# Optimization experiments

Measured on AMD Instinct MI355X. Metric: run time of the kernel, lower is better.

Reference implementation:

```python
import jax, jax.numpy as jnp
import numpy as np

D = 128   # hidden_dims
H = 8     # head_num
ALPHA = 0.5
EPS = 1e-5


def setup_inputs() -> dict:
    key = jax.random.key(0)
    ks = jax.random.split(key, 16)
    B, S = 2, 2048
    s = 0.02
    inp = {
        'x': jax.random.normal(ks[0], (B, S, D), jnp.float32),
        'adj_matrix': jax.random.randint(ks[1], (S, S), 0, 2, jnp.int32),
        'Wq': jax.random.normal(ks[2], (D, D * H), jnp.float32) * s,
        'bq': jnp.zeros((D * H,), jnp.float32),
        'Wk': jax.random.normal(ks[3], (D, D * H), jnp.float32) * s,
        'bk': jnp.zeros((D * H,), jnp.float32),
        'Wv': jax.random.normal(ks[4], (D, D * H), jnp.float32) * s,
        'bv': jnp.zeros((D * H,), jnp.float32),
        'Wo': jax.random.normal(ks[5], (D * H, D), jnp.float32) * s,
        'bo': jnp.zeros((D,), jnp.float32),
        'g1': jnp.ones((D,), jnp.float32), 'be1': jnp.zeros((D,), jnp.float32),
        'g2': jnp.ones((D,), jnp.float32), 'be2': jnp.zeros((D,), jnp.float32),
        'W1': jax.random.normal(ks[6], (D, D), jnp.float32) * s,
        'b1': jnp.zeros((D,), jnp.float32),
        'W2': jax.random.normal(ks[7], (D, D), jnp.float32) * s,
        'b2': jnp.zeros((D,), jnp.float32),
    }
    return inp


def _layernorm(x, g, b):
    mu = jnp.mean(x, axis=-1, keepdims=True)
    var = jnp.var(x, axis=-1, keepdims=True)
    return (x - mu) * jax.lax.rsqrt(var + EPS) * g + b


def reference(x, adj_matrix, Wq, bq, Wk, bk, Wv, bv, Wo, bo, g1, be1, g2, be2, W1, b1, W2, b2):
    B, S, _ = x.shape
    q = (x @ Wq + bq).reshape(B, S, H, D)
    k = (x @ Wk + bk).reshape(B, S, H, D)
    v = (x @ Wv + bv).reshape(B, S, H, D)
    scores = jnp.einsum('bqhd,bkhd->bhqk', q, k) / jnp.sqrt(jnp.float32(D))
    soft_mask = ALPHA * adj_matrix.astype(jnp.float32) + (1.0 - ALPHA)  # [S,S]
    scores = scores * soft_mask  # broadcast over B,H
    attn = jax.nn.softmax(scores, axis=-1)
    out = jnp.einsum('bhqk,bkhd->bqhd', attn, v).reshape(B, S, H * D)
    out = out @ Wo + bo
    h = _layernorm(x + out, g1, be1)
    ff = jax.nn.relu(h @ W1 + b1) @ W2 + b2
    y = _layernorm(h + ff, g2, be2)
    return y, attn
```

## Files before the change

kernel.cpp:

```cpp
#include <hip/hip_runtime.h>
#include <hip/hip_bf16.h>

#define HD 128
#define NH 8
#define SQ 2048
#define NROWS 4096
#define QSCALE 0.06375871607f

typedef __bf16 bf16;
typedef bf16 bf16x8 __attribute__((ext_vector_type(8)));
typedef float f32x4 __attribute__((ext_vector_type(4)));

__device__ __forceinline__ f32x4 mfma16(bf16x8 a, bf16x8 b, f32x4 c) {
  return __builtin_amdgcn_mfma_f32_16x16x32_bf16(a, b, c, 0, 0, 0);
}
__device__ __forceinline__ bf16x8 ld8(const bf16* p) { return *(const bf16x8*)p; }
__device__ __forceinline__ unsigned short bfu(float v) {
  return __builtin_bit_cast(unsigned short, (bf16)v);
}
__device__ __forceinline__ unsigned packbf2(float a, float b) {
  return (unsigned)bfu(a) | ((unsigned)bfu(b) << 16);
}
__device__ __forceinline__ void gload_lds16(const void* g, void* l) {
  __builtin_amdgcn_global_load_lds(
      (const __attribute__((address_space(1))) void*)g,
      (__attribute__((address_space(3))) void*)l, 16, 0, 0);
}

__global__ void k_prep_a(const float* __restrict__ x, const int* __restrict__ adj,
                         bf16* __restrict__ xb, unsigned char* __restrict__ mask8) {
  int idx = blockIdx.x * 256 + threadIdx.x;
  if (idx < NROWS * HD) { xb[idx] = (bf16)x[idx]; return; }
  int j = idx - NROWS * HD;
  if (j < (SQ * SQ / 4)) {
    int4 a = ((const int4*)adj)[j];
    uchar4 m;
    m.x = (unsigned char)a.x; m.y = (unsigned char)a.y;
    m.z = (unsigned char)a.z; m.w = (unsigned char)a.w;
    ((uchar4*)mask8)[j] = m;
  }
}

__global__ void k_prep_w(const float* __restrict__ Wq, const float* __restrict__ Wk,
                         const float* __restrict__ Wv, const float* __restrict__ Wo,
                         const float* __restrict__ W1, const float* __restrict__ W2,
                         bf16* __restrict__ WqkvT, bf16* __restrict__ WoT,
                         bf16* __restrict__ W1T, bf16* __restrict__ W2T) {
  int idx = blockIdx.x * 256 + threadIdx.x;
  if (idx < 3072 * 128) {
    int n = idx >> 7, kk = idx & 127;
    int sel = n >> 10, nn = n & 1023;
    const float* W = (sel == 0) ? Wq : (sel == 1 ? Wk : Wv);
    WqkvT[idx] = (bf16)W[kk * 1024 + nn];
    return;
  }
  int j = idx - 3072 * 128;
  if (j < 128 * 1024) { int n = j >> 10, kk = j & 1023; WoT[j] = (bf16)Wo[kk * 128 + n]; return; }
  j -= 128 * 1024;
  if (j < 16384) { int n = j >> 7, kk = j & 127; W1T[j] = (bf16)W1[kk * 128 + n]; return; }
  j -= 16384;
  if (j < 16384) { int n = j >> 7, kk = j & 127; W2T[j] = (bf16)W2[kk * 128 + n]; return; }
}

__global__ __launch_bounds__(256, 4) void k_qkv(
    const bf16* __restrict__ xb, const bf16* __restrict__ WqkvT,
    const float* __restrict__ bq, const float* __restrict__ bk, const float* __restrict__ bv,
    bf16* __restrict__ qT, bf16* __restrict__ kT, bf16* __restrict__ vT) {
  const int bid = blockIdx.x;
  const int m0 = (bid & 63) << 6;
  const int n0 = (bid >> 6) << 6;
  const int tid = threadIdx.x;
  const int w = tid >> 6, lane = tid & 63, lo = lane & 15, hi = lane >> 4;
  const int mw = m0 + ((w >> 1) << 5);
  const int nw = n0 + ((w & 1) << 5);
  bf16x8 av[2][4], bw[2][4];
#pragma unroll
  for (int ms = 0; ms < 2; ++ms)
#pragma unroll
    for (int ks = 0; ks < 4; ++ks)
      av[ms][ks] = ld8(xb + (size_t)(mw + ms * 16 + lo) * 128 + ks * 32 + hi * 8);
#pragma unroll
  for (int ns = 0; ns < 2; ++ns)
#pragma unroll
    for (int ks = 0; ks < 4; ++ks)
      bw[ns][ks] = ld8(WqkvT + (size_t)(nw + ns * 16 + lo) * 128 + ks * 32 + hi * 8);
  const f32x4 z4 = {0.f, 0.f, 0.f, 0.f};
  f32x4 acc[2][2] = {{z4, z4}, {z4, z4}};
#pragma unroll
  for (int ms = 0; ms < 2; ++ms)
#pragma unroll
    for (int ns = 0; ns < 2; ++ns)
#pragma unroll
      for (int ks = 0; ks < 4; ++ks)
        acc[ms][ns] = mfma16(av[ms][ks], bw[ns][ks], acc[ms][ns]);
#pragma unroll
  for (int ns = 0; ns < 2; ++ns) {
    const int n = nw + ns * 16 + lo;
    const int sel = n >> 10, nn = n & 1023;
    const float bia = (sel == 0 ? bq : sel == 1 ? bk : bv)[nn];
    const int hh = nn >> 7, d = nn & 127;
#pragma unroll
    for (int ms = 0; ms < 2; ++ms) {
      const int mb = mw + ms * 16 + hi * 4;
      const int bb = mb >> 11, s = mb & 2047;
      if (sel == 0) {
#pragma unroll
        for (int r = 0; r < 4; ++r)
          qT[(size_t)((bb * 8 + hh) * 2048 + s + r) * 128 + d] =
              (bf16)((acc[ms][ns][r] + bia) * QSCALE);
      } else if (sel == 1) {
#pragma unroll
        for (int r = 0; r < 4; ++r)
          kT[(size_t)((bb * 8 + hh) * 2048 + s + r) * 128 + d] = (bf16)(acc[ms][ns][r] + bia);
      } else {
        ushort4 pk;
        pk.x = bfu(acc[ms][ns][0] + bia);
        pk.y = bfu(acc[ms][ns][1] + bia);
        pk.z = bfu(acc[ms][ns][2] + bia);
        pk.w = bfu(acc[ms][ns][3] + bia);
        *(ushort4*)(vT + (size_t)((bb * 8 + hh) * 128 + d) * 2048 + s) = pk;
      }
    }
  }
}

__global__ __launch_bounds__(256, 2) void k_attn(
    const bf16* __restrict__ qT, const bf16* __restrict__ kT,
    const bf16* __restrict__ vT, const unsigned char* __restrict__ mask8,
    float* __restrict__ attn_out, bf16* __restrict__ Oc) {
  __shared__ __align__(16) char kbuf[2][8192];
  __shared__ __align__(16) char vbuf[2][8192];
  __shared__ __align__(16) char stash[4][1024];
  __shared__ float red2[64];

  const int lbid = blockIdx.x;
  const int work = ((lbid & 7) << 6) + (lbid >> 3);
  const int bh = work >> 5;
  const int q0 = (work & 31) << 6;
  const int b = bh >> 3, h = bh & 7;
  const int tid = threadIdx.x;
  const int w = tid >> 6, lane = tid & 63, lo = lane & 15, hi = lane >> 4;

  const bf16* Qh = qT + (size_t)bh * SQ * HD;
  const bf16* Kh = kT + (size_t)bh * SQ * HD;
  const bf16* Vh = vT + (size_t)bh * HD * SQ;
  const int qg = q0 + w * 16 + lo;

  const int krow0 = (w << 2) + (lane >> 4);
  const int krow1 = 16 + krow0;
  const bf16* kg0 = Kh + (size_t)krow0 * HD + (((lane & 15) ^ (krow0 & 7)) << 3);
  const bf16* kg1 = Kh + (size_t)krow1 * HD + (((lane & 15) ^ (krow1 & 7)) << 3);
  const int vrow0 = (w << 4) + (lane >> 2);
  const int vrow1 = 64 + vrow0;
  const bf16* vg0 = Vh + (size_t)vrow0 * SQ + ((lane & 3) << 3);
  const bf16* vg1 = Vh + (size_t)vrow1 * SQ + ((lane & 3) << 3);

  bf16x8 qf[4];
#pragma unroll
  for (int ks = 0; ks < 4; ++ks)
    qf[ks] = ld8(Qh + (size_t)qg * HD + ks * 32 + hi * 8);

  const f32x4 z4 = {0.f, 0.f, 0.f, 0.f};
  f32x4 acc[8];
#pragma unroll
  for (int ds = 0; ds < 8; ++ds) acc[ds] = z4;
  float ssum = 0.f;

  gload_lds16(kg0, &kbuf[0][w * 1024]);
  gload_lds16(kg1, &kbuf[0][4096 + w * 1024]);
  gload_lds16(vg0, &vbuf[0][w * 1024]);
  gload_lds16(vg1, &vbuf[0][4096 + w * 1024]);
  __syncthreads();

  for (int i = 0; i < 64; ++i) {
    const int kvA = i << 5;
    const int cur = i & 1;
    if (i < 63) {
      const size_t ko = (size_t)(kvA + 32) * HD;
      gload_lds16(kg0 + ko, &kbuf[cur ^ 1][w * 1024]);
      gload_lds16(kg1 + ko, &kbuf[cur ^ 1][4096 + w * 1024]);
      gload_lds16(vg0 + (kvA + 32), &vbuf[cur ^ 1][w * 1024]);
      gload_lds16(vg1 + (kvA + 32), &vbuf[cur ^ 1][4096 + w * 1024]);
    }
    const char* kb = kbuf[cur];
    const char* vb = vbuf[cur];
#pragma unroll
    for (int t = 0; t < 2; ++t) {
      const int row = t * 16 + lo;
      bf16x8 af[4];
#pragma unroll
      for (int ks = 0; ks < 4; ++ks)
        af[ks] = *(const bf16x8*)(kb + row * 256 + ((((ks << 2) + hi)) ^ (row & 7)) * 16);
      f32x4 c = z4;
#pragma unroll
      for (int ks = 0; ks < 4; ++ks) c = mfma16(af[ks], qf[ks], c);
      const unsigned mu = *(const unsigned*)(mask8 + (size_t)qg * SQ + kvA + t * 16 + hi * 4);
      float p0 = exp2f(fmaf(c[0], (float)(mu & 0xff),         c[0]));
      float p1 = exp2f(fmaf(c[1], (float)((mu >> 8) & 0xff),  c[1]));
      float p2 = exp2f(fmaf(c[2], (float)((mu >> 16) & 0xff), c[2]));
      float p3 = exp2f(fmaf(c[3], (float)((mu >> 24) & 0xff), c[3]));
      ssum += (p0 + p1) + (p2 + p3);
      *(uint2*)(stash[w] + lo * 64 + ((t * 32 + hi * 8) ^ ((lo & 3) << 4))) =
          make_uint2(packbf2(p0, p1), packbf2(p2, p3));
    }
    bf16x8 pa = *(const bf16x8*)(stash[w] + lo * 64 + ((hi * 16) ^ ((lo & 3) << 4)));
    __builtin_amdgcn_s_setprio(1);
#pragma unroll
    for (int ds = 0; ds < 8; ++ds) {
      bf16x8 vf = *(const bf16x8*)(vb + (ds * 16 + lo) * 64 + hi * 16);
      acc[ds] = mfma16(pa, vf, acc[ds]);
    }
    __builtin_amdgcn_s_setprio(0);
    __syncthreads();
  }

  ssum += __shfl_xor(ssum, 16);
  ssum += __shfl_xor(ssum, 32);
  if (hi == 0) red2[w * 16 + lo] = 1.0f / ssum;
  __syncthreads();

#pragma unroll
  for (int ds = 0; ds < 8; ++ds)
#pragma unroll
    for (int r = 0; r < 4; ++r) {
      const int qrow = w * 16 + hi * 4 + r;
      Oc[(size_t)(b * SQ + q0 + qrow) * (NH * HD) + h * HD + ds * 16 + lo] =
          (bf16)(acc[ds][r] * red2[qrow]);
    }

  const float lr = log2f(red2[w * 16 + lo]);
  float* abase = attn_out + (size_t)bh * SQ * SQ + (size_t)qg * SQ;
  gload_lds16(kg0, &kbuf[0][w * 1024]);
  gload_lds16(kg1, &kbuf[0][4096 + w * 1024]);
  __syncthreads();
  for (int i = 0; i < 64; ++i) {
    const int kvA = i << 5;
    const int cur = i & 1;
    if (i < 63) {
      const size_t ko = (size_t)(kvA + 32) * HD;
      gload_lds16(kg0 + ko, &kbuf[cur ^ 1][w * 1024]);
      gload_lds16(kg1 + ko, &kbuf[cur ^ 1][4096 + w * 1024]);
    }
    const char* kb = kbuf[cur];
#pragma unroll
    for (int t = 0; t < 2; ++t) {
      const int row = t * 16 + lo;
      bf16x8 af[4];
#pragma unroll
      for (int ks = 0; ks < 4; ++ks)
        af[ks] = *(const bf16x8*)(kb + row * 256 + ((((ks << 2) + hi)) ^ (row & 7)) * 16);
      f32x4 c = z4;
#pragma unroll
      for (int ks = 0; ks < 4; ++ks) c = mfma16(af[ks], qf[ks], c);
      const unsigned mu = *(const unsigned*)(mask8 + (size_t)qg * SQ + kvA + t * 16 + hi * 4);
      f32x4 o;
      o[0] = exp2f(fmaf(c[0], (float)(mu & 0xff),         c[0] + lr));
      o[1] = exp2f(fmaf(c[1], (float)((mu >> 8) & 0xff),  c[1] + lr));
      o[2] = exp2f(fmaf(c[2], (float)((mu >> 16) & 0xff), c[2] + lr));
      o[3] = exp2f(fmaf(c[3], (float)((mu >> 24) & 0xff), c[3] + lr));
      __builtin_nontemporal_store(o, (f32x4*)(abase + kvA + t * 16 + hi * 4));
    }
    __syncthreads();
  }
}

__global__ __launch_bounds__(256, 4) void k_owo(
    const bf16* __restrict__ Oc, const bf16* __restrict__ WoT,
    const float* __restrict__ bo, const float* __restrict__ x,
    const float* __restrict__ g1, const float* __restrict__ be1,
    float* __restrict__ hf, bf16* __restrict__ hb) {
  __shared__ __align__(16) float hbuf[16 * 128];
  const int m0 = blockIdx.x * 16;
  const int tid = threadIdx.x;
  const int w = tid >> 6, lane = tid & 63, lo = lane & 15, hi = lane >> 4;
  const int nw = w * 32;
  const f32x4 z4 = {0.f, 0.f, 0.f, 0.f};
  f32x4 acc[2] = {z4, z4};
#pragma unroll 4
  for (int kk = 0; kk < 32; ++kk) {
    bf16x8 a = ld8(Oc + (size_t)(m0 + lo) * 1024 + kk * 32 + hi * 8);
#pragma unroll
    for (int ns = 0; ns < 2; ++ns) {
      bf16x8 bb = ld8(WoT + (size_t)(nw + ns * 16 + lo) * 1024 + kk * 32 + hi * 8);
      acc[ns] = mfma16(a, bb, acc[ns]);
    }
  }
#pragma unroll
  for (int ns = 0; ns < 2; ++ns) {
    const int n = nw + ns * 16 + lo;
    const float bia = bo[n];
#pragma unroll
    for (int r = 0; r < 4; ++r) {
      const int mr = hi * 4 + r;
      hbuf[mr * 128 + n] = acc[ns][r] + bia + x[(size_t)(m0 + mr) * 128 + n];
    }
  }
  __syncthreads();
  const float2 g = *(const float2*)(g1 + lane * 2);
  const float2 be = *(const float2*)(be1 + lane * 2);
#pragma unroll
  for (int rr = 0; rr < 4; ++rr) {
    const int row = w * 4 + rr;
    float2 v = *(float2*)&hbuf[row * 128 + lane * 2];
    float s = v.x + v.y, sq = v.x * v.x + v.y * v.y;
#pragma unroll
    for (int off = 32; off; off >>= 1) { s += __shfl_xor(s, off); sq += __shfl_xor(sq, off); }
    const float mean = s * (1.f / 128.f);
    const float var = sq * (1.f / 128.f) - mean * mean;
    const float rstd = rsqrtf(var + 1e-5f);
    const float y0 = (v.x - mean) * rstd * g.x + be.x;
    const float y1 = (v.y - mean) * rstd * g.y + be.y;
    const size_t o = (size_t)(m0 + row) * 128 + lane * 2;
    *(float2*)(hf + o) = make_float2(y0, y1);
    *(unsigned*)(hb + o) = packbf2(y0, y1);
  }
}

__global__ __launch_bounds__(256, 4) void k_ffn(
    const bf16* __restrict__ hb, const float* __restrict__ hf,
    const bf16* __restrict__ W1T, const bf16* __restrict__ W2T,
    const float* __restrict__ b1, const float* __restrict__ b2,
    const float* __restrict__ g2, const float* __restrict__ be2,
    float* __restrict__ yout) {
  __shared__ __align__(16) bf16 s1[16 * 136];
  __shared__ __align__(16) float ybuf[16 * 128];
  const int m0 = blockIdx.x * 16;
  const int tid = threadIdx.x;
  const int w = tid >> 6, lane = tid & 63, lo = lane & 15, hi = lane >> 4;
  const int nw = w * 32;
  const f32x4 z4 = {0.f, 0.f, 0.f, 0.f};
  f32x4 a1[2] = {z4, z4};
#pragma unroll
  for (int kk = 0; kk < 4; ++kk) {
    bf16x8 a = ld8(hb + (size_t)(m0 + lo) * 128 + kk * 32 + hi * 8);
#pragma unroll
    for (int ns = 0; ns < 2; ++ns)
      a1[ns] = mfma16(a, ld8(W1T + (size_t)(nw + ns * 16 + lo) * 128 + kk * 32 + hi * 8), a1[ns]);
  }
#pragma unroll
  for (int ns = 0; ns < 2; ++ns) {
    const int n = nw + ns * 16 + lo;
    const float bia = b1[n];
#pragma unroll
    for (int r = 0; r < 4; ++r)
      s1[(hi * 4 + r) * 136 + n] = (bf16)fmaxf(a1[ns][r] + bia, 0.f);
  }
  __syncthreads();
  f32x4 a2[2] = {z4, z4};
#pragma unroll
  for (int kk = 0; kk < 4; ++kk) {
    bf16x8 a = *(const bf16x8*)&s1[lo * 136 + kk * 32 + hi * 8];
#pragma unroll
    for (int ns = 0; ns < 2; ++ns)
      a2[ns] = mfma16(a, ld8(W2T + (size_t)(nw + ns * 16 + lo) * 128 + kk * 32 + hi * 8), a2[ns]);
  }
#pragma unroll
  for (int ns = 0; ns < 2; ++ns) {
    const int n = nw + ns * 16 + lo;
    const float bia = b2[n];
#pragma unroll
    for (int r = 0; r < 4; ++r) {
      const int mr = hi * 4 + r;
      ybuf[mr * 128 + n] = a2[ns][r] + bia + hf[(size_t)(m0 + mr) * 128 + n];
    }
  }
  __syncthreads();
  const float2 g = *(const float2*)(g2 + lane * 2);
  const float2 be = *(const float2*)(be2 + lane * 2);
#pragma unroll
  for (int rr = 0; rr < 4; ++rr) {
    const int row = w * 4 + rr;
    float2 v = *(float2*)&ybuf[row * 128 + lane * 2];
    float s = v.x + v.y, sq = v.x * v.x + v.y * v.y;
#pragma unroll
    for (int off = 32; off; off >>= 1) { s += __shfl_xor(s, off); sq += __shfl_xor(sq, off); }
    const float mean = s * (1.f / 128.f);
    const float var = sq * (1.f / 128.f) - mean * mean;
    const float rstd = rsqrtf(var + 1e-5f);
    const float y0 = (v.x - mean) * rstd * g.x + be.x;
    const float y1 = (v.y - mean) * rstd * g.y + be.y;
    *(float2*)(yout + (size_t)(m0 + row) * 128 + lane * 2) = make_float2(y0, y1);
  }
}

extern "C" void kernel_launch(void* const* d_in, const int* in_sizes, int n_in,
                              void* d_out, int out_size, void* d_ws, size_t ws_size,
                              hipStream_t stream) {
  const float* x  = (const float*)d_in[0];
  const int* adj  = (const int*)d_in[1];
  const float* Wq = (const float*)d_in[2];  const float* bq = (const float*)d_in[3];
  const float* Wk = (const float*)d_in[4];  const float* bk = (const float*)d_in[5];
  const float* Wv = (const float*)d_in[6];  const float* bv = (const float*)d_in[7];
  const float* Wo = (const float*)d_in[8];  const float* bo = (const float*)d_in[9];
  const float* g1 = (const float*)d_in[10]; const float* be1 = (const float*)d_in[11];
  const float* g2 = (const float*)d_in[12]; const float* be2 = (const float*)d_in[13];
  const float* W1 = (const float*)d_in[14]; const float* b1 = (const float*)d_in[15];
  const float* W2 = (const float*)d_in[16]; const float* b2 = (const float*)d_in[17];

  char* ws = (char*)d_ws;
  bf16* xb     = (bf16*)(ws + 0);
  bf16* WqkvT  = (bf16*)(ws + 1048576);
  bf16* WoT    = (bf16*)(ws + 1835008);
  bf16* W1T    = (bf16*)(ws + 2097152);
  bf16* W2T    = (bf16*)(ws + 2129920);
  unsigned char* mask8 = (unsigned char*)(ws + 2162688);
  bf16* qT     = (bf16*)(ws + 6356992);
  bf16* kT     = (bf16*)(ws + 14745600);
  bf16* vT     = (bf16*)(ws + 23134208);
  bf16* Oc     = (bf16*)(ws + 31522816);
  float* hf    = (float*)(ws + 39911424);
  bf16* hb     = (bf16*)(ws + 42008576);

  float* yout = (float*)d_out;
  float* attn_out = yout + (size_t)NROWS * HD;

  k_prep_a<<<6144, 256, 0, stream>>>(x, adj, xb, mask8);
  k_prep_w<<<2176, 256, 0, stream>>>(Wq, Wk, Wv, Wo, W1, W2, WqkvT, WoT, W1T, W2T);
  k_qkv<<<3072, 256, 0, stream>>>(xb, WqkvT, bq, bk, bv, qT, kT, vT);
  k_attn<<<512, 256, 0, stream>>>(qT, kT, vT, mask8, attn_out, Oc);
  k_owo<<<256, 256, 0, stream>>>(Oc, WoT, bo, x, g1, be1, hf, hb);
  k_ffn<<<256, 256, 0, stream>>>(hb, hf, W1T, W2T, b1, b2, g2, be2, yout);
}
```

Before: 211.7 us.

## Split attention blocks to 32 query rows with two waves per block

The attention kernel now runs 1024 blocks of 128 threads, each handling 32 query rows instead of 64, and K/V tile staging is redistributed so each of the two waves loads four 1KB chunks. The aim is better occupancy and load balance across CUs, since 512 blocks of 256 threads may underfill the GPU. In exchange, each block loads K/V tiles for half as many queries, which doubles total K/V traffic from L2.

```diff
diff --git a/kernel.cpp b/kernel.cpp
--- a/kernel.cpp
+++ b/kernel.cpp
@@ -124,19 +124,19 @@
   }
 }
 
-__global__ __launch_bounds__(256, 2) void k_attn(
+__global__ __launch_bounds__(128, 2) void k_attn(
     const bf16* __restrict__ qT, const bf16* __restrict__ kT,
     const bf16* __restrict__ vT, const unsigned char* __restrict__ mask8,
     float* __restrict__ attn_out, bf16* __restrict__ Oc) {
   __shared__ __align__(16) char kbuf[2][8192];
   __shared__ __align__(16) char vbuf[2][8192];
-  __shared__ __align__(16) char stash[4][1024];
-  __shared__ float red2[64];
+  __shared__ __align__(16) char stash[2][1024];
+  __shared__ float red2[32];
 
   const int lbid = blockIdx.x;
-  const int work = ((lbid & 7) << 6) + (lbid >> 3);
-  const int bh = work >> 5;
-  const int q0 = (work & 31) << 6;
+  const int work = ((lbid & 7) << 7) + (lbid >> 3);
+  const int bh = work >> 6;
+  const int q0 = (work & 63) << 5;
   const int b = bh >> 3, h = bh & 7;
   const int tid = threadIdx.x;
   const int w = tid >> 6, lane = tid & 63, lo = lane & 15, hi = lane >> 4;
@@ -146,14 +146,25 @@
   const bf16* Vh = vT + (size_t)bh * HD * SQ;
   const int qg = q0 + w * 16 + lo;
 
-  const int krow0 = (w << 2) + (lane >> 4);
-  const int krow1 = 16 + krow0;
-  const bf16* kg0 = Kh + (size_t)krow0 * HD + (((lane & 15) ^ (krow0 & 7)) << 3);
-  const bf16* kg1 = Kh + (size_t)krow1 * HD + (((lane & 15) ^ (krow1 & 7)) << 3);
-  const int vrow0 = (w << 4) + (lane >> 2);
-  const int vrow1 = 64 + vrow0;
-  const bf16* vg0 = Vh + (size_t)vrow0 * SQ + ((lane & 3) << 3);
-  const bf16* vg1 = Vh + (size_t)vrow1 * SQ + ((lane & 3) << 3);
+  const int rit = lane >> 4;
+  const bf16* kgA = Kh + (size_t)(w * 16 + rit) * HD + (((lane & 15) ^ rit) << 3);
+  const bf16* kgB = Kh + (size_t)(w * 16 + rit) * HD + (((lane & 15) ^ (4 + rit)) << 3);
+  const bf16* vg  = Vh + (size_t)(w * 64 + (lane >> 2)) * SQ + ((lane & 3) << 3);
+  char* kdst = (char*)0;
+  auto stageK = [&](char* kb, int kvbase) {
+    char* base = kb + w * 4096;
+    gload_lds16(kgA + (size_t)(kvbase + 0) * HD,  base + 0 * 1024);
+    gload_lds16(kgB + (size_t)(kvbase + 4) * HD,  base + 1 * 1024);
+    gload_lds16(kgA + (size_t)(kvbase + 8) * HD,  base + 2 * 1024);
+    gload_lds16(kgB + (size_t)(kvbase + 12) * HD, base + 3 * 1024);
+  };
+  auto stageV = [&](char* vb, int kvbase) {
+    char* base = vb + w * 4096;
+    gload_lds16(vg + (size_t)(0 * 16) * SQ + kvbase, base + 0 * 1024);
+    gload_lds16(vg + (size_t)(1 * 16) * SQ + kvbase, base + 1 * 1024);
+    gload_lds16(vg + (size_t)(2 * 16) * SQ + kvbase, base + 2 * 1024);
+    gload_lds16(vg + (size_t)(3 * 16) * SQ + kvbase, base + 3 * 1024);
+  };
 
   bf16x8 qf[4];
 #pragma unroll
@@ -166,21 +177,16 @@
   for (int ds = 0; ds < 8; ++ds) acc[ds] = z4;
   float ssum = 0.f;
 
-  gload_lds16(kg0, &kbuf[0][w * 1024]);
-  gload_lds16(kg1, &kbuf[0][4096 + w * 1024]);
-  gload_lds16(vg0, &vbuf[0][w * 1024]);
-  gload_lds16(vg1, &vbuf[0][4096 + w * 1024]);
+  stageK(kbuf[0], 0);
+  stageV(vbuf[0], 0);
   __syncthreads();
 
   for (int i = 0; i < 64; ++i) {
     const int kvA = i << 5;
     const int cur = i & 1;
     if (i < 63) {
-      const size_t ko = (size_t)(kvA + 32) * HD;
-      gload_lds16(kg0 + ko, &kbuf[cur ^ 1][w * 1024]);
-      gload_lds16(kg1 + ko, &kbuf[cur ^ 1][4096 + w * 1024]);
-      gload_lds16(vg0 + (kvA + 32), &vbuf[cur ^ 1][w * 1024]);
-      gload_lds16(vg1 + (kvA + 32), &vbuf[cur ^ 1][4096 + w * 1024]);
+      stageK(kbuf[cur ^ 1], kvA + 32);
+      stageV(vbuf[cur ^ 1], kvA + 32);
     }
     const char* kb = kbuf[cur];
     const char* vb = vbuf[cur];
@@ -230,17 +236,12 @@
 
   const float lr = log2f(red2[w * 16 + lo]);
   float* abase = attn_out + (size_t)bh * SQ * SQ + (size_t)qg * SQ;
-  gload_lds16(kg0, &kbuf[0][w * 1024]);
-  gload_lds16(kg1, &kbuf[0][4096 + w * 1024]);
+  stageK(kbuf[0], 0);
   __syncthreads();
   for (int i = 0; i < 64; ++i) {
     const int kvA = i << 5;
     const int cur = i & 1;
-    if (i < 63) {
-      const size_t ko = (size_t)(kvA + 32) * HD;
-      gload_lds16(kg0 + ko, &kbuf[cur ^ 1][w * 1024]);
-      gload_lds16(kg1 + ko, &kbuf[cur ^ 1][4096 + w * 1024]);
-    }
+    if (i < 63) stageK(kbuf[cur ^ 1], kvA + 32);
     const char* kb = kbuf[cur];
 #pragma unroll
     for (int t = 0; t < 2; ++t) {
@@ -417,7 +418,7 @@
   k_prep_a<<<6144, 256, 0, stream>>>(x, adj, xb, mask8);
   k_prep_w<<<2176, 256, 0, stream>>>(Wq, Wk, Wv, Wo, W1, W2, WqkvT, WoT, W1T, W2T);
   k_qkv<<<3072, 256, 0, stream>>>(xb, WqkvT, bq, bk, bv, qT, kT, vT);
-  k_attn<<<512, 256, 0, stream>>>(qT, kT, vT, mask8, attn_out, Oc);
+  k_attn<<<1024, 128, 0, stream>>>(qT, kT, vT, mask8, attn_out, Oc);
   k_owo<<<256, 256, 0, stream>>>(Oc, WoT, bo, x, g1, be1, hf, hb);
   k_ffn<<<256, 256, 0, stream>>>(hb, hf, W1T, W2T, b1, b2, g2, be2, yout);
 }
```

Measured after the change: 228.7 us. 1.08x slower.
